# Performance work log

Hardware: AMD Instinct MI355X
Metric: run time of the kernel (lower is better)

## Reference

```python
import jax, jax.numpy as jnp
import numpy as np

KS = 64      # kernel_size
NFFT = 64    # n_fft
IC = 32      # in_channel
OC = 64      # out_channel
B, T1, T2 = 4, 4096, 512


def setup_inputs() -> dict:
    key = jax.random.key(0)
    k1, k2, k3, k4 = jax.random.split(key, 4)
    x = jax.random.normal(k1, (B, T1, IC), dtype=jnp.float32)
    # continuous index in [0, T1-1)
    index = jax.random.uniform(k2, (B, T2), dtype=jnp.float32) * (T1 - 1)
    kb = 1.0 / np.sqrt(KS * IC)  # matches reset_parameters uniform bound
    kernel = jax.random.uniform(k3, (OC, IC, NFFT), minval=-kb, maxval=kb, dtype=jnp.float32)
    bias = jax.random.uniform(k4, (OC,), minval=-kb, maxval=kb, dtype=jnp.float32)
    return {"x": x, "index": index, "kernel": kernel, "bias": bias}


def reference(x, index, kernel, bias):
    # fractional-delay kernel per (b, t2) via FFT phase shift
    i = jnp.floor(index).astype(jnp.int32)          # (b, t2) integer part
    f = index - jnp.floor(index)                    # (b, t2) fractional part
    freqs = jnp.arange(NFFT // 2 + 1)               # rfft bins
    shift = jnp.exp(2j * jnp.pi * f[..., None] * freqs / NFFT)   # (b, t2, nf)
    K = jnp.fft.rfft(kernel)                        # (oc, ic, nf)
    K = K[None, None] * shift[:, :, None, None, :]  # (b, t2, oc, ic, nf)
    ker = jnp.fft.irfft(K, n=KS)                    # (b, t2, oc, ic, ks)

    # gather centered length-ks windows of x at integer positions i
    pad = KS // 2
    x_pad = jnp.pad(x, ((0, 0), (pad, pad), (0, 0)))            # (b, t1+2p, ic)
    pos = i[:, :, None] + jnp.arange(KS)[None, None, :]          # (b, t2, ks)
    barr = jnp.arange(x.shape[0])[:, None, None]
    xwin = x_pad[barr, pos]                                      # (b, t2, ks, ic)

    # per-position matmul: out[b,t,o] = sum_{c,k} ker[b,t,o,c,k] * xwin[b,t,k,c]
    out = jnp.einsum('btock,btkc->bto', ker, xwin) + bias
    return out
```

## Files before the change

kernel.cpp:

```cpp
#include <hip/hip_runtime.h>
#include <hip/hip_bf16.h>
#include <math.h>

#define B_   4
#define T1_  4096
#define T2_  512
#define IC_  32
#define OC_  64
#define KS_  64

typedef unsigned short u16;
typedef unsigned int   u32;

__device__ __forceinline__ float bf2f(u16 h) {
    union { u32 u; float f; } v; v.u = ((u32)h) << 16; return v.f;
}
__device__ __forceinline__ u16 f2bf(float f) {
    union { u32 u; float f; } v; v.f = f;
    u32 u = v.u;
    u32 r = (u + 0x7FFFu + ((u >> 16) & 1u)) >> 16;
    return (u16)r;
}

#define PI_F 3.14159265358979323846f

__global__ __launch_bounds__(256) void prep_kernel(const float* __restrict__ kern,
                                                   float* __restrict__ KT)
{
    int gid = blockIdx.x * 256 + threadIdx.x;
    int o   = gid >> 9;
    int cs4 = gid & 511;
    float4 v = *(const float4*)(kern + (size_t)o * 2048 + (cs4 << 2));
    *(float4*)(KT + ((size_t)cs4 * 64 + o) * 4) = v;
}

__global__ __launch_bounds__(256) void interp_kernel(const float* __restrict__ x,
                                                     const float* __restrict__ index,
                                                     u16* __restrict__ Y)
{
    __shared__ __align__(16) float xwT[IC_][68];
    __shared__ float wsh[64];

    const int bt  = blockIdx.x;
    const int b   = bt >> 9;
    const int tid = threadIdx.x;

    float fidx = index[bt];
    float flo  = floorf(fidx);
    int   i0   = (int)flo;
    float f    = fidx - flo;

    {
        int e  = tid * 8;
        int k  = e >> 5;
        int c0 = e & 31;
        int pos = i0 + k - 32;
        float vals[8];
        if (pos >= 0 && pos < T1_) {
            const float* p = x + ((size_t)(b * T1_ + pos) * IC_ + c0);
            float4 a = *(const float4*)p;
            float4 d = *(const float4*)(p + 4);
            vals[0]=a.x; vals[1]=a.y; vals[2]=a.z; vals[3]=a.w;
            vals[4]=d.x; vals[5]=d.y; vals[6]=d.z; vals[7]=d.w;
        } else {
            #pragma unroll
            for (int q = 0; q < 8; ++q) vals[q] = 0.0f;
        }
        #pragma unroll
        for (int q = 0; q < 8; ++q) xwT[c0 + q][k] = vals[q];
    }

    if (tid < 64) {
        int j = tid;
        float wj;
        if (f <= 0.0f) {
            wj = (j == 0) ? 1.0f : 0.0f;
        } else {
            float spf = sinf(PI_F * f);
            float a   = PI_F * ((float)j + f) * (1.0f / 64.0f);
            float sa  = sinf(a);
            float ca  = cosf(a);
            wj = ((j & 1) ? -spf : spf) * ca / (64.0f * sa);
        }
        wsh[j] = wj;
    }
    __syncthreads();

    const int c  = tid >> 3;
    const int s0 = (tid & 7) << 3;

    float xr[64];
    #pragma unroll
    for (int q = 0; q < 16; ++q) {
        int idx = (s0 + q * 4) & 63;
        const float4 v = *(const float4*)&xwT[c][idx];
        xr[q*4+0] = v.x; xr[q*4+1] = v.y; xr[q*4+2] = v.z; xr[q*4+3] = v.w;
    }

    float acc[8];
    #pragma unroll
    for (int r = 0; r < 8; ++r) acc[r] = 0.0f;

    #pragma unroll
    for (int j = 0; j < 64; ++j) {
        float wj = wsh[j];
        #pragma unroll
        for (int r = 0; r < 8; ++r)
            acc[r] += wj * xr[(j + r) & 63];
    }

    u16 ov[8];
    #pragma unroll
    for (int r = 0; r < 8; ++r) ov[r] = f2bf(acc[r]);
    u16* yp = Y + ((size_t)bt * 2048 + c * 64 + s0);
    *(ushort4*)(yp)     = make_ushort4(ov[0], ov[1], ov[2], ov[3]);
    *(ushort4*)(yp + 4) = make_ushort4(ov[4], ov[5], ov[6], ov[7]);
}

__global__ __launch_bounds__(256) void gemm_kernel(const u16* __restrict__ Y,
                                                   const float* __restrict__ KT,
                                                   const float* __restrict__ bias,
                                                   float* __restrict__ out)
{
    __shared__ __align__(16) float Ylds[4][2048];
    __shared__ float red[4][4][64];

    const int tid = threadIdx.x;
    const int bt0 = blockIdx.x * 4;

    #pragma unroll
    for (int it = 0; it < 4; ++it) {
        int e   = (it * 256 + tid) * 8;
        int row = e >> 11;
        int col = e & 2047;
        const u16* p = Y + ((size_t)(bt0 + row) * 2048 + col);
        ushort4 a = *(const ushort4*)p;
        ushort4 d = *(const ushort4*)(p + 4);
        Ylds[row][col+0]=bf2f(a.x); Ylds[row][col+1]=bf2f(a.y);
        Ylds[row][col+2]=bf2f(a.z); Ylds[row][col+3]=bf2f(a.w);
        Ylds[row][col+4]=bf2f(d.x); Ylds[row][col+5]=bf2f(d.y);
        Ylds[row][col+6]=bf2f(d.z); Ylds[row][col+7]=bf2f(d.w);
    }
    __syncthreads();

    const int o  = tid & 63;
    const int kq = tid >> 6;

    float acc0 = 0.f, acc1 = 0.f, acc2 = 0.f, acc3 = 0.f;

    for (int i2 = 0; i2 < 128; ++i2) {
        int cs4 = kq * 128 + i2;
        float4 kv = *(const float4*)(KT + ((size_t)cs4 * 64 + o) * 4);
        int cc = cs4 * 4;
        float4 y0 = *(const float4*)&Ylds[0][cc];
        float4 y1 = *(const float4*)&Ylds[1][cc];
        float4 y2 = *(const float4*)&Ylds[2][cc];
        float4 y3 = *(const float4*)&Ylds[3][cc];
        acc0 += kv.x*y0.x + kv.y*y0.y + kv.z*y0.z + kv.w*y0.w;
        acc1 += kv.x*y1.x + kv.y*y1.y + kv.z*y1.z + kv.w*y1.w;
        acc2 += kv.x*y2.x + kv.y*y2.y + kv.z*y2.z + kv.w*y2.w;
        acc3 += kv.x*y3.x + kv.y*y3.y + kv.z*y3.z + kv.w*y3.w;
    }

    red[kq][0][o] = acc0;
    red[kq][1][o] = acc1;
    red[kq][2][o] = acc2;
    red[kq][3][o] = acc3;
    __syncthreads();

    {
        int r  = tid >> 6;
        int oo = tid & 63;
        float s = red[0][r][oo] + red[1][r][oo] + red[2][r][oo] + red[3][r][oo]
                + bias[oo];
        out[(size_t)(bt0 + r) * 64 + oo] = s;
    }
}

extern "C" void kernel_launch(void* const* d_in, const int* in_sizes, int n_in,
                              void* d_out, int out_size, void* d_ws, size_t ws_size,
                              hipStream_t stream)
{
    const float* x     = (const float*)d_in[0];
    const float* index = (const float*)d_in[1];
    const float* kern  = (const float*)d_in[2];
    const float* bias  = (const float*)d_in[3];
    float* out = (float*)d_out;

    u16*   Y  = (u16*)d_ws;
    float* KT = (float*)((char*)d_ws + (size_t)8 * 1024 * 1024);

    prep_kernel<<<dim3(128), dim3(256), 0, stream>>>(kern, KT);
    interp_kernel<<<dim3(B_ * T2_), dim3(256), 0, stream>>>(x, index, Y);
    gemm_kernel<<<dim3(B_ * T2_ / 4), dim3(256), 0, stream>>>(Y, KT, bias, out);
}
```

Before: 89.64 us.

## Use bf16 MFMA for the channel-kernel GEMM with pre-swizzled bf16 weights

Replaces the fp32 LDS-staged dot-product GEMM with a single-wave kernel that runs mfma_f32_16x16x32_bf16 over 16 rows and all 64 outputs. The weight tensor is converted to bf16 in the prep kernel and laid out to match the MFMA B-operand fragment. Operand loads come straight from global memory and are software-prefetched one K step ahead. The interp kernel also reads its weights as float4. Weights lose precision by going to bf16, and with only 128 single-wave blocks the GEMM may underuse the GPU.

```diff
diff --git a/kernel.cpp b/kernel.cpp
--- a/kernel.cpp
+++ b/kernel.cpp
@@ -11,6 +11,8 @@
 
 typedef unsigned short u16;
 typedef unsigned int   u32;
+typedef __attribute__((ext_vector_type(8))) short  short8;
+typedef __attribute__((ext_vector_type(4))) float  float4v;
 
 __device__ __forceinline__ float bf2f(u16 h) {
     union { u32 u; float f; } v; v.u = ((u32)h) << 16; return v.f;
@@ -25,13 +27,17 @@
 #define PI_F 3.14159265358979323846f
 
 __global__ __launch_bounds__(256) void prep_kernel(const float* __restrict__ kern,
-                                                   float* __restrict__ KT)
+                                                   u16* __restrict__ Bsz)
 {
     int gid = blockIdx.x * 256 + threadIdx.x;
-    int o   = gid >> 9;
-    int cs4 = gid & 511;
-    float4 v = *(const float4*)(kern + (size_t)o * 2048 + (cs4 << 2));
-    *(float4*)(KT + ((size_t)cs4 * 64 + o) * 4) = v;
+    int o   = gid & 63;
+    int cs8 = gid >> 6;
+    const float* p = kern + (size_t)o * 2048 + cs8 * 8;
+    float4 a = *(const float4*)p;
+    float4 b = *(const float4*)(p + 4);
+    u16* q = Bsz + (size_t)cs8 * 512 + o * 8;
+    *(ushort4*)(q)     = make_ushort4(f2bf(a.x), f2bf(a.y), f2bf(a.z), f2bf(a.w));
+    *(ushort4*)(q + 4) = make_ushort4(f2bf(b.x), f2bf(b.y), f2bf(b.z), f2bf(b.w));
 }
 
 __global__ __launch_bounds__(256) void interp_kernel(const float* __restrict__ x,
@@ -39,7 +45,7 @@
                                                      u16* __restrict__ Y)
 {
     __shared__ __align__(16) float xwT[IC_][68];
-    __shared__ float wsh[64];
+    __shared__ __align__(16) float wsh[64];
 
     const int bt  = blockIdx.x;
     const int b   = bt >> 9;
@@ -102,11 +108,16 @@
     for (int r = 0; r < 8; ++r) acc[r] = 0.0f;
 
     #pragma unroll
-    for (int j = 0; j < 64; ++j) {
-        float wj = wsh[j];
+    for (int jq = 0; jq < 16; ++jq) {
+        const float4 wv = *(const float4*)&wsh[jq * 4];
         #pragma unroll
-        for (int r = 0; r < 8; ++r)
-            acc[r] += wj * xr[(j + r) & 63];
+        for (int jj = 0; jj < 4; ++jj) {
+            const float wj = (jj == 0) ? wv.x : (jj == 1) ? wv.y : (jj == 2) ? wv.z : wv.w;
+            const int j = jq * 4 + jj;
+            #pragma unroll
+            for (int r = 0; r < 8; ++r)
+                acc[r] += wj * xr[(j + r) & 63];
+        }
     }
 
     u16 ov[8];
@@ -117,63 +128,60 @@
     *(ushort4*)(yp + 4) = make_ushort4(ov[4], ov[5], ov[6], ov[7]);
 }
 
-__global__ __launch_bounds__(256) void gemm_kernel(const u16* __restrict__ Y,
-                                                   const float* __restrict__ KT,
-                                                   const float* __restrict__ bias,
-                                                   float* __restrict__ out)
-{
-    __shared__ __align__(16) float Ylds[4][2048];
-    __shared__ float red[4][4][64];
-
-    const int tid = threadIdx.x;
-    const int bt0 = blockIdx.x * 4;
-
-    #pragma unroll
-    for (int it = 0; it < 4; ++it) {
-        int e   = (it * 256 + tid) * 8;
-        int row = e >> 11;
-        int col = e & 2047;
-        const u16* p = Y + ((size_t)(bt0 + row) * 2048 + col);
-        ushort4 a = *(const ushort4*)p;
-        ushort4 d = *(const ushort4*)(p + 4);
-        Ylds[row][col+0]=bf2f(a.x); Ylds[row][col+1]=bf2f(a.y);
-        Ylds[row][col+2]=bf2f(a.z); Ylds[row][col+3]=bf2f(a.w);
-        Ylds[row][col+4]=bf2f(d.x); Ylds[row][col+5]=bf2f(d.y);
-        Ylds[row][col+6]=bf2f(d.z); Ylds[row][col+7]=bf2f(d.w);
-    }
-    __syncthreads();
-
-    const int o  = tid & 63;
-    const int kq = tid >> 6;
-
-    float acc0 = 0.f, acc1 = 0.f, acc2 = 0.f, acc3 = 0.f;
-
-    for (int i2 = 0; i2 < 128; ++i2) {
-        int cs4 = kq * 128 + i2;
-        float4 kv = *(const float4*)(KT + ((size_t)cs4 * 64 + o) * 4);
-        int cc = cs4 * 4;
-        float4 y0 = *(const float4*)&Ylds[0][cc];
-        float4 y1 = *(const float4*)&Ylds[1][cc];
-        float4 y2 = *(const float4*)&Ylds[2][cc];
-        float4 y3 = *(const float4*)&Ylds[3][cc];
-        acc0 += kv.x*y0.x + kv.y*y0.y + kv.z*y0.z + kv.w*y0.w;
-        acc1 += kv.x*y1.x + kv.y*y1.y + kv.z*y1.z + kv.w*y1.w;
-        acc2 += kv.x*y2.x + kv.y*y2.y + kv.z*y2.z + kv.w*y2.w;
-        acc3 += kv.x*y3.x + kv.y*y3.y + kv.z*y3.z + kv.w*y3.w;
-    }
-
-    red[kq][0][o] = acc0;
-    red[kq][1][o] = acc1;
-    red[kq][2][o] = acc2;
-    red[kq][3][o] = acc3;
-    __syncthreads();
-
-    {
-        int r  = tid >> 6;
-        int oo = tid & 63;
-        float s = red[0][r][oo] + red[1][r][oo] + red[2][r][oo] + red[3][r][oo]
-                + bias[oo];
-        out[(size_t)(bt0 + r) * 64 + oo] = s;
+__global__ __launch_bounds__(64) void gemm_kernel(const u16* __restrict__ Y,
+                                                  const u16* __restrict__ Bsz,
+                                                  const float* __restrict__ bias,
+                                                  float* __restrict__ out)
+{
+    const int lane = threadIdx.x;
+    const int nm   = lane & 15;
+    const int q    = lane >> 4;
+    const int bt0  = blockIdx.x * 16;
+
+    float4v acc0 = {0.f, 0.f, 0.f, 0.f};
+    float4v acc1 = {0.f, 0.f, 0.f, 0.f};
+    float4v acc2 = {0.f, 0.f, 0.f, 0.f};
+    float4v acc3 = {0.f, 0.f, 0.f, 0.f};
+
+    const u16* aptr = Y   + (size_t)(bt0 + nm) * 2048 + q * 8;
+    const u16* bptr = Bsz + (size_t)q * 512 + nm * 8;
+
+    short8 a  = *(const short8*)(aptr);
+    short8 b0 = *(const short8*)(bptr);
+    short8 b1 = *(const short8*)(bptr + 128);
+    short8 b2 = *(const short8*)(bptr + 256);
+    short8 b3 = *(const short8*)(bptr + 384);
+
+    for (int kb = 0; kb < 64; ++kb) {
+        short8 an, bn0, bn1, bn2, bn3;
+        if (kb != 63) {
+            const u16* ap = aptr + (kb + 1) * 32;
+            const u16* bp = bptr + (size_t)(kb + 1) * 2048;
+            an  = *(const short8*)(ap);
+            bn0 = *(const short8*)(bp);
+            bn1 = *(const short8*)(bp + 128);
+            bn2 = *(const short8*)(bp + 256);
+            bn3 = *(const short8*)(bp + 384);
+        }
+        acc0 = __builtin_amdgcn_mfma_f32_16x16x32_bf16(a, b0, acc0, 0, 0, 0);
+        acc1 = __builtin_amdgcn_mfma_f32_16x16x32_bf16(a, b1, acc1, 0, 0, 0);
+        acc2 = __builtin_amdgcn_mfma_f32_16x16x32_bf16(a, b2, acc2, 0, 0, 0);
+        acc3 = __builtin_amdgcn_mfma_f32_16x16x32_bf16(a, b3, acc3, 0, 0, 0);
+        if (kb != 63) { a = an; b0 = bn0; b1 = bn1; b2 = bn2; b3 = bn3; }
+    }
+
+    const float bs0 = bias[nm];
+    const float bs1 = bias[16 + nm];
+    const float bs2 = bias[32 + nm];
+    const float bs3 = bias[48 + nm];
+    #pragma unroll
+    for (int r = 0; r < 4; ++r) {
+        const int row = bt0 + q * 4 + r;
+        float* op = out + (size_t)row * 64 + nm;
+        op[0]  = acc0[r] + bs0;
+        op[16] = acc1[r] + bs1;
+        op[32] = acc2[r] + bs2;
+        op[48] = acc3[r] + bs3;
     }
 }
 
@@ -187,10 +195,10 @@
     const float* bias  = (const float*)d_in[3];
     float* out = (float*)d_out;
 
-    u16*   Y  = (u16*)d_ws;
-    float* KT = (float*)((char*)d_ws + (size_t)8 * 1024 * 1024);
-
-    prep_kernel<<<dim3(128), dim3(256), 0, stream>>>(kern, KT);
+    u16* Y   = (u16*)d_ws;
+    u16* Bsz = (u16*)((char*)d_ws + (size_t)8 * 1024 * 1024);
+
+    prep_kernel<<<dim3(64),  dim3(256), 0, stream>>>(kern, Bsz);
     interp_kernel<<<dim3(B_ * T2_), dim3(256), 0, stream>>>(x, index, Y);
-    gemm_kernel<<<dim3(B_ * T2_ / 4), dim3(256), 0, stream>>>(Y, KT, bias, out);
-}
+    gemm_kernel<<<dim3(B_ * T2_ / 16), dim3(64), 0, stream>>>(Y, Bsz, bias, out);
+}
```

New measurement: 102.5 us. 14.3% more time.
